# Performance work log

Measured on AMD Instinct MI355X. Metric: run time of the kernel, lower is better.

The kernel has to match this reference:

```python
import jax, jax.numpy as jnp
import numpy as np

N_VOX = 200000   # active input voxels
M_VOX = 100000   # active output voxels
K_VOL = 27       # 3x3x3 kernel offsets
C_IN = 32
C_OUT = 64


def setup_inputs() -> dict:
    key = jax.random.key(0)
    k1, k2, k3, k4 = jax.random.split(key, 4)
    feats = jax.random.normal(k1, (N_VOX, C_IN), dtype=jnp.float32)
    # kernel init ~ U(-std, std), std = 1/sqrt(in_channels * kernel_volume)
    std = 1.0 / np.sqrt(C_IN * K_VOL)
    kernel = jax.random.uniform(k2, (K_VOL, C_IN, C_OUT), dtype=jnp.float32,
                                minval=-std, maxval=std)
    # kernel map: for each offset k and output voxel m, an input voxel index
    in_idx = jax.random.randint(k3, (K_VOL, M_VOX), 0, N_VOX, dtype=jnp.int32)
    # occupancy mask: 1 if that (offset, output) pair exists in the kernel map
    mask = jax.random.randint(k4, (K_VOL, M_VOX), 0, 2, dtype=jnp.int32)
    return {"feats": feats, "kernel": kernel, "in_idx": in_idx, "mask": mask}


def reference(feats, kernel, in_idx, mask) -> jnp.ndarray:
    # Gather neighbor features per kernel offset: [K, M, C_in]
    gathered = feats[in_idx]
    gathered = gathered * mask[..., None].astype(feats.dtype)
    # Per-offset GEMM + scatter-add (offsets align on output voxels, so the
    # scatter-add is a sum over the K axis): [M, C_out]
    out = jnp.einsum('kmi,kio->mo', gathered, kernel)
    return out
```

## Files before the change

### kernel.cpp

```cpp
#include <hip/hip_runtime.h>

#define M_VOX   100000
#define N_VOX   200000
#define K_VOL   27
#define C_IN    32
#define C_OUT   64

typedef __bf16 bf16x8 __attribute__((ext_vector_type(8)));
typedef float  floatx4 __attribute__((ext_vector_type(4)));

#define FEATSB_BYTES  ((N_VOX + 1) * C_IN * 2)
#define BFRAG_OFF     FEATSB_BYTES
#define BFRAG_BYTES   (K_VOL * 256 * 16)
#define MIDX_OFF      (BFRAG_OFF + BFRAG_BYTES)

__global__ __launch_bounds__(256) void prep_feats(
    const float* __restrict__ feats, __bf16* __restrict__ featsB)
{
    const int c = blockIdx.x * 256 + threadIdx.x;
    const int nchunk = (N_VOX + 1) * 4;
    if (c >= nchunk) return;
    bf16x8 v;
    if (c < N_VOX * 4) {
        floatx4 f0 = *(const floatx4*)(feats + c * 8);
        floatx4 f1 = *(const floatx4*)(feats + c * 8 + 4);
#pragma unroll
        for (int j = 0; j < 4; ++j) { v[j] = (__bf16)f0[j]; v[4 + j] = (__bf16)f1[j]; }
    } else {
#pragma unroll
        for (int j = 0; j < 8; ++j) v[j] = (__bf16)0.0f;
    }
    *(bf16x8*)(featsB + c * 8) = v;
}

__global__ __launch_bounds__(256) void prep_weights(
    const float* __restrict__ kernelw, bf16x8* __restrict__ Bfrag)
{
    const int k    = blockIdx.x;
    const int tid  = threadIdx.x;
    const int tile = tid >> 6;
    const int col  = tid & 15;
    const int quad = (tid >> 4) & 3;
    const float* kp = kernelw + k * C_IN * C_OUT + quad * 8 * C_OUT + tile * 16 + col;
    bf16x8 b;
#pragma unroll
    for (int j = 0; j < 8; ++j) b[j] = (__bf16)kp[j * C_OUT];
    Bfrag[k * 256 + tid] = b;
}

__global__ __launch_bounds__(256) void prep_midx(
    const int* __restrict__ in_idx, const int* __restrict__ mask,
    int* __restrict__ midx)
{
    const int t = blockIdx.x * 256 + threadIdx.x;
    const int4 i4 = ((const int4*)in_idx)[t];
    const int4 m4 = ((const int4*)mask)[t];
    int4 o;
    o.x = m4.x ? i4.x : N_VOX;
    o.y = m4.y ? i4.y : N_VOX;
    o.z = m4.z ? i4.z : N_VOX;
    o.w = m4.w ? i4.w : N_VOX;
    ((int4*)midx)[t] = o;
}

__global__ __launch_bounds__(256) void sparse_conv_mfma(
    const __bf16* __restrict__ featsB,
    const bf16x8* __restrict__ Bfrag,
    const int* __restrict__ midx,
    float* __restrict__ out)
{
    const int tid  = threadIdx.x;
    const int lane = tid & 63;
    const int wv   = tid >> 6;
    const int col  = lane & 15;
    const int quad = lane >> 4;

    const int m0 = blockIdx.x * 64 + wv * 16;
    if (m0 >= M_VOX) return;

    int mi[K_VOL];
#pragma unroll
    for (int k = 0; k < K_VOL; ++k) mi[k] = midx[k * M_VOX + m0 + col];

    floatx4 acc0 = {0.f,0.f,0.f,0.f}, acc1 = {0.f,0.f,0.f,0.f};
    floatx4 acc2 = {0.f,0.f,0.f,0.f}, acc3 = {0.f,0.f,0.f,0.f};

    const bf16x8* bbase = Bfrag + lane;

    bf16x8 a_n  = *(const bf16x8*)(featsB + (long)mi[0] * C_IN + quad * 8);
    bf16x8 b0_n = bbase[0*64], b1_n = bbase[1*64], b2_n = bbase[2*64], b3_n = bbase[3*64];

#pragma unroll
    for (int k = 0; k < K_VOL; ++k) {
        bf16x8 a = a_n, b0 = b0_n, b1 = b1_n, b2 = b2_n, b3 = b3_n;
        if (k + 1 < K_VOL) {
            a_n = *(const bf16x8*)(featsB + (long)mi[k + 1] * C_IN + quad * 8);
            const bf16x8* bb = bbase + (k + 1) * 256;
            b0_n = bb[0*64]; b1_n = bb[1*64]; b2_n = bb[2*64]; b3_n = bb[3*64];
        }
        acc0 = __builtin_amdgcn_mfma_f32_16x16x32_bf16(a, b0, acc0, 0, 0, 0);
        acc1 = __builtin_amdgcn_mfma_f32_16x16x32_bf16(a, b1, acc1, 0, 0, 0);
        acc2 = __builtin_amdgcn_mfma_f32_16x16x32_bf16(a, b2, acc2, 0, 0, 0);
        acc3 = __builtin_amdgcn_mfma_f32_16x16x32_bf16(a, b3, acc3, 0, 0, 0);
    }

    float* op = out + (long)(m0 + quad * 4) * C_OUT + col;
#pragma unroll
    for (int r = 0; r < 4; ++r) {
        op[r * C_OUT + 0]  = acc0[r];
        op[r * C_OUT + 16] = acc1[r];
        op[r * C_OUT + 32] = acc2[r];
        op[r * C_OUT + 48] = acc3[r];
    }
}

extern "C" void kernel_launch(void* const* d_in, const int* in_sizes, int n_in,
                              void* d_out, int out_size, void* d_ws, size_t ws_size,
                              hipStream_t stream) {
    const float* feats   = (const float*)d_in[0];
    const float* kernelw = (const float*)d_in[1];
    const int*   in_idx  = (const int*)d_in[2];
    const int*   maskp   = (const int*)d_in[3];
    float*       out     = (float*)d_out;

    __bf16* featsB = (__bf16*)d_ws;
    bf16x8* BfragP = (bf16x8*)((char*)d_ws + BFRAG_OFF);
    int*    midxP  = (int*)((char*)d_ws + MIDX_OFF);

    {
        const int nchunk = (N_VOX + 1) * 4;
        prep_feats<<<dim3((nchunk + 255) / 256), dim3(256), 0, stream>>>(feats, featsB);
    }
    prep_weights<<<dim3(K_VOL), dim3(256), 0, stream>>>(kernelw, BfragP);
    {
        const int nthr = K_VOL * M_VOX / 4;
        prep_midx<<<dim3(nthr / 256 + 1), dim3(256), 0, stream>>>(in_idx, maskp, midxP);
    }

    const int blocks = (M_VOX + 63) / 64;
    sparse_conv_mfma<<<dim3(blocks), dim3(256), 0, stream>>>(featsB, BfragP, midxP, out);
}
```

Measured before the change: 138.1 us.

## Fuse prep kernels, fold mask into main kernel, deepen gather prefetch

```diff
diff --git a/kernel.cpp b/kernel.cpp
--- a/kernel.cpp
+++ b/kernel.cpp
@@ -5,68 +5,53 @@
 #define K_VOL   27
 #define C_IN    32
 #define C_OUT   64
+#define DEPTH   14
 
 typedef __bf16 bf16x8 __attribute__((ext_vector_type(8)));
 typedef float  floatx4 __attribute__((ext_vector_type(4)));
 
 #define FEATSB_BYTES  ((N_VOX + 1) * C_IN * 2)
 #define BFRAG_OFF     FEATSB_BYTES
-#define BFRAG_BYTES   (K_VOL * 256 * 16)
-#define MIDX_OFF      (BFRAG_OFF + BFRAG_BYTES)
 
-__global__ __launch_bounds__(256) void prep_feats(
-    const float* __restrict__ feats, __bf16* __restrict__ featsB)
+#define FEAT_CHUNKS   ((N_VOX + 1) * 4)
+#define FEAT_BLOCKS   ((FEAT_CHUNKS + 255) / 256)
+__global__ __launch_bounds__(256) void prep_all(
+    const float* __restrict__ feats, const float* __restrict__ kernelw,
+    __bf16* __restrict__ featsB, bf16x8* __restrict__ Bfrag)
 {
-    const int c = blockIdx.x * 256 + threadIdx.x;
-    const int nchunk = (N_VOX + 1) * 4;
-    if (c >= nchunk) return;
-    bf16x8 v;
-    if (c < N_VOX * 4) {
-        floatx4 f0 = *(const floatx4*)(feats + c * 8);
-        floatx4 f1 = *(const floatx4*)(feats + c * 8 + 4);
+    if (blockIdx.x < FEAT_BLOCKS) {
+        const int c = blockIdx.x * 256 + threadIdx.x;
+        if (c >= FEAT_CHUNKS) return;
+        bf16x8 v;
+        if (c < N_VOX * 4) {
+            floatx4 f0 = *(const floatx4*)(feats + c * 8);
+            floatx4 f1 = *(const floatx4*)(feats + c * 8 + 4);
 #pragma unroll
-        for (int j = 0; j < 4; ++j) { v[j] = (__bf16)f0[j]; v[4 + j] = (__bf16)f1[j]; }
+            for (int j = 0; j < 4; ++j) { v[j] = (__bf16)f0[j]; v[4 + j] = (__bf16)f1[j]; }
+        } else {
+#pragma unroll
+            for (int j = 0; j < 8; ++j) v[j] = (__bf16)0.0f;
+        }
+        *(bf16x8*)(featsB + c * 8) = v;
     } else {
+        const int k    = blockIdx.x - FEAT_BLOCKS;
+        const int tid  = threadIdx.x;
+        const int tile = tid >> 6;
+        const int col  = tid & 15;
+        const int quad = (tid >> 4) & 3;
+        const float* kp = kernelw + k * C_IN * C_OUT + quad * 8 * C_OUT + tile * 16 + col;
+        bf16x8 b;
 #pragma unroll
-        for (int j = 0; j < 8; ++j) v[j] = (__bf16)0.0f;
+        for (int j = 0; j < 8; ++j) b[j] = (__bf16)kp[j * C_OUT];
+        Bfrag[k * 256 + tid] = b;
     }
-    *(bf16x8*)(featsB + c * 8) = v;
 }
 
-__global__ __launch_bounds__(256) void prep_weights(
-    const float* __restrict__ kernelw, bf16x8* __restrict__ Bfrag)
-{
-    const int k    = blockIdx.x;
-    const int tid  = threadIdx.x;
-    const int tile = tid >> 6;
-    const int col  = tid & 15;
-    const int quad = (tid >> 4) & 3;
-    const float* kp = kernelw + k * C_IN * C_OUT + quad * 8 * C_OUT + tile * 16 + col;
-    bf16x8 b;
-#pragma unroll
-    for (int j = 0; j < 8; ++j) b[j] = (__bf16)kp[j * C_OUT];
-    Bfrag[k * 256 + tid] = b;
-}
-
-__global__ __launch_bounds__(256) void prep_midx(
-    const int* __restrict__ in_idx, const int* __restrict__ mask,
-    int* __restrict__ midx)
-{
-    const int t = blockIdx.x * 256 + threadIdx.x;
-    const int4 i4 = ((const int4*)in_idx)[t];
-    const int4 m4 = ((const int4*)mask)[t];
-    int4 o;
-    o.x = m4.x ? i4.x : N_VOX;
-    o.y = m4.y ? i4.y : N_VOX;
-    o.z = m4.z ? i4.z : N_VOX;
-    o.w = m4.w ? i4.w : N_VOX;
-    ((int4*)midx)[t] = o;
-}
-
-__global__ __launch_bounds__(256) void sparse_conv_mfma(
+__global__ __launch_bounds__(256, 3) void sparse_conv_mfma(
     const __bf16* __restrict__ featsB,
     const bf16x8* __restrict__ Bfrag,
-    const int* __restrict__ midx,
+    const int* __restrict__ in_idx,
+    const int* __restrict__ mask,
     float* __restrict__ out)
 {
     const int tid  = threadIdx.x;
@@ -80,31 +65,45 @@
 
     int mi[K_VOL];
 #pragma unroll
-    for (int k = 0; k < K_VOL; ++k) mi[k] = midx[k * M_VOX + m0 + col];
+    for (int k = 0; k < K_VOL; ++k) {
+        const int ix = in_idx[k * M_VOX + m0 + col];
+        const int mk = mask[k * M_VOX + m0 + col];
+        mi[k] = mk ? ix : N_VOX;
+    }
+
+    const __bf16* fbase = featsB + quad * 8;
+
+    bf16x8 A[DEPTH];
+#pragma unroll
+    for (int k = 0; k < DEPTH; ++k)
+        A[k] = *(const bf16x8*)(fbase + (size_t)mi[k] * C_IN);
 
     floatx4 acc0 = {0.f,0.f,0.f,0.f}, acc1 = {0.f,0.f,0.f,0.f};
     floatx4 acc2 = {0.f,0.f,0.f,0.f}, acc3 = {0.f,0.f,0.f,0.f};
 
     const bf16x8* bbase = Bfrag + lane;
-
-    bf16x8 a_n  = *(const bf16x8*)(featsB + (long)mi[0] * C_IN + quad * 8);
-    bf16x8 b0_n = bbase[0*64], b1_n = bbase[1*64], b2_n = bbase[2*64], b3_n = bbase[3*64];
+    bf16x8 nb0 = bbase[0*64], nb1 = bbase[1*64], nb2 = bbase[2*64], nb3 = bbase[3*64];
 
 #pragma unroll
     for (int k = 0; k < K_VOL; ++k) {
-        bf16x8 a = a_n, b0 = b0_n, b1 = b1_n, b2 = b2_n, b3 = b3_n;
+        const int s = k % DEPTH;
+        bf16x8 a  = A[s];
+        bf16x8 b0 = nb0, b1 = nb1, b2 = nb2, b3 = nb3;
+
+        if (k + DEPTH < K_VOL)
+            A[s] = *(const bf16x8*)(fbase + (size_t)mi[k + DEPTH] * C_IN);
         if (k + 1 < K_VOL) {
-            a_n = *(const bf16x8*)(featsB + (long)mi[k + 1] * C_IN + quad * 8);
             const bf16x8* bb = bbase + (k + 1) * 256;
-            b0_n = bb[0*64]; b1_n = bb[1*64]; b2_n = bb[2*64]; b3_n = bb[3*64];
+            nb0 = bb[0*64]; nb1 = bb[1*64]; nb2 = bb[2*64]; nb3 = bb[3*64];
         }
+
         acc0 = __builtin_amdgcn_mfma_f32_16x16x32_bf16(a, b0, acc0, 0, 0, 0);
         acc1 = __builtin_amdgcn_mfma_f32_16x16x32_bf16(a, b1, acc1, 0, 0, 0);
         acc2 = __builtin_amdgcn_mfma_f32_16x16x32_bf16(a, b2, acc2, 0, 0, 0);
         acc3 = __builtin_amdgcn_mfma_f32_16x16x32_bf16(a, b3, acc3, 0, 0, 0);
     }
 
-    float* op = out + (long)(m0 + quad * 4) * C_OUT + col;
+    float* op = out + (size_t)(m0 + quad * 4) * C_OUT + col;
 #pragma unroll
     for (int r = 0; r < 4; ++r) {
         op[r * C_OUT + 0]  = acc0[r];
@@ -125,18 +124,11 @@
 
     __bf16* featsB = (__bf16*)d_ws;
     bf16x8* BfragP = (bf16x8*)((char*)d_ws + BFRAG_OFF);
-    int*    midxP  = (int*)((char*)d_ws + MIDX_OFF);
 
-    {
-        const int nchunk = (N_VOX + 1) * 4;
-        prep_feats<<<dim3((nchunk + 255) / 256), dim3(256), 0, stream>>>(feats, featsB);
-    }
-    prep_weights<<<dim3(K_VOL), dim3(256), 0, stream>>>(kernelw, BfragP);
-    {
-        const int nthr = K_VOL * M_VOX / 4;
-        prep_midx<<<dim3(nthr / 256 + 1), dim3(256), 0, stream>>>(in_idx, maskp, midxP);
-    }
+    prep_all<<<dim3(FEAT_BLOCKS + K_VOL), dim3(256), 0, stream>>>(
+        feats, kernelw, featsB, BfragP);
 
     const int blocks = (M_VOX + 63) / 64;
-    sparse_conv_mfma<<<dim3(blocks), dim3(256), 0, stream>>>(featsB, BfragP, midxP, out);
+    sparse_conv_mfma<<<dim3(blocks), dim3(256), 0, stream>>>(
+        featsB, BfragP, in_idx, maskp, out);
 }
```

New measurement: 137.2 us. About the same (-0.7%).
